# Kernel tuning notes

Measured on AMD Instinct MI355X. Metric: run time of the kernel, lower is better.

Reference implementation:

```python
import jax, jax.numpy as jnp
import numpy as np

B, P, D = 16384, 4096, 256

def setup_inputs() -> dict:
    key = jax.random.key(0)
    kx, kp = jax.random.split(key)
    x = jax.random.normal(kx, (B, D), dtype=jnp.float32)
    prototypes = jax.random.normal(kp, (P, D), dtype=jnp.float32)
    return {"x": x, "prototypes": prototypes}

def reference(x, prototypes):
    # Pairwise L2 distance: ||x - p||_2 for every (batch, prototype) pair.
    # GEMM reformulation avoids the O(B*P*D) broadcast intermediate:
    x_sq = jnp.sum(x * x, axis=-1, keepdims=True)                 # [B, 1]
    p_sq = jnp.sum(prototypes * prototypes, axis=-1)[None, :]     # [1, P]
    xp = jnp.einsum('bd,pd->bp', x, prototypes)                   # [B, P]
    sq_dist = jnp.maximum(x_sq + p_sq - 2.0 * xp, 0.0)
    return jnp.sqrt(sq_dist)                                      # [B, P]
```

## Files before the change

kernel.cpp:

```cpp
#include <hip/hip_runtime.h>
#include <hip/hip_bf16.h>

#define B_DIM 16384
#define P_DIM 4096
#define D_DIM 256
#define BK 32
#define NSTEP (D_DIM / BK)

typedef float f32x4 __attribute__((ext_vector_type(4)));
typedef __bf16 bf16x8 __attribute__((ext_vector_type(8)));

__device__ __forceinline__ unsigned short f2bf_rne(float f) {
  unsigned int u = __builtin_bit_cast(unsigned int, f);
  u += 0x7fffu + ((u >> 16) & 1u);
  return (unsigned short)(u >> 16);
}

__global__ __launch_bounds__(256) void prep_kernel(
    const float* __restrict__ x, const float* __restrict__ p,
    unsigned short* __restrict__ xb, unsigned short* __restrict__ pb,
    float* __restrict__ xsq, float* __restrict__ psq) {
  int row  = blockIdx.x * 4 + (threadIdx.x >> 6);
  int lane = threadIdx.x & 63;
  const float4* src;
  unsigned short* dst;
  float* sq;
  if (row < B_DIM) {
    src = (const float4*)(x + (size_t)row * D_DIM);
    dst = xb + (size_t)row * D_DIM;
    sq  = xsq + row;
  } else {
    int r = row - B_DIM;
    src = (const float4*)(p + (size_t)r * D_DIM);
    dst = pb + (size_t)r * D_DIM;
    sq  = psq + r;
  }
  float4 v = src[lane];
  ushort4 o;
  o.x = f2bf_rne(v.x); o.y = f2bf_rne(v.y);
  o.z = f2bf_rne(v.z); o.w = f2bf_rne(v.w);
  ((ushort4*)dst)[lane] = o;
  float s = v.x * v.x + v.y * v.y + v.z * v.z + v.w * v.w;
  #pragma unroll
  for (int off = 32; off > 0; off >>= 1) s += __shfl_down(s, off);
  if (lane == 0) *sq = s;
}

__device__ __forceinline__ void async16(const unsigned short* g, const void* l) {
  __builtin_amdgcn_global_load_lds(
      (const __attribute__((address_space(1))) void*)g,
      (__attribute__((address_space(3))) void*)l,
      16, 0, 0);
}

__global__ __launch_bounds__(256, 3) void dist_gemm(
    const unsigned short* __restrict__ A,
    const unsigned short* __restrict__ Bm,
    const float* __restrict__ xsq, const float* __restrict__ psq,
    float* __restrict__ out) {
  __shared__ __align__(16) char lds[3][2][8192];

  const int tid  = threadIdx.x;
  const int w    = tid >> 6;
  const int lane = tid & 63;
  const int bid  = blockIdx.x;

  const int swz = (bid & 7) * 512 + (bid >> 3);
  const int bm  = swz >> 5;
  const int bn  = swz & 31;

  const int wr = w >> 1;
  const int wc = w & 1;

  const int trow = tid >> 2;
  const int tcol = (((tid & 3) ^ (trow & 3)) << 3);
  const unsigned short* aSrc = A  + (size_t)(bm * 128 + trow) * D_DIM + tcol;
  const unsigned short* bSrc = Bm + (size_t)(bn * 128 + trow) * D_DIM + tcol;
  const int ldst = tid * 16;

#define STAGE(bufi, ktE) do { _Pragma("unroll")                                \
    for (int i = 0; i < 2; ++i) {                                              \
      async16(aSrc + (size_t)i * 64 * D_DIM + (ktE),                           \
              (const void*)(&lds[bufi][0][0] + i * 4096 + ldst));              \
      async16(bSrc + (size_t)i * 64 * D_DIM + (ktE),                           \
              (const void*)(&lds[bufi][1][0] + i * 4096 + ldst));              \
    } } while (0)

  const int arow = wr * 64 + (lane & 15);
  const int brow = wc * 64 + (lane & 15);
  const int koff = (((lane >> 4) ^ (lane & 3)) << 4);

  f32x4 acc[4][4];
  #pragma unroll
  for (int m = 0; m < 4; ++m)
    #pragma unroll
    for (int n = 0; n < 4; ++n) acc[m][n] = 0.0f;

  STAGE(0, 0);
  STAGE(1, BK);

  #pragma unroll
  for (int t = 0; t < NSTEP; ++t) {
    if (t < NSTEP - 1) asm volatile("s_waitcnt vmcnt(4)" ::: "memory");
    else               asm volatile("s_waitcnt vmcnt(0)" ::: "memory");
    __builtin_amdgcn_s_barrier();
    __builtin_amdgcn_sched_barrier(0);

    if (t < NSTEP - 2) {
      const int nb = (t + 2) % 3;
      STAGE(nb, (t + 2) * BK);
    }

    const char* La = &lds[t % 3][0][0];
    const char* Lb = &lds[t % 3][1][0];
    bf16x8 av[4], bv[4];
    #pragma unroll
    for (int m = 0; m < 4; ++m)
      av[m] = *(const bf16x8*)(La + (arow + m * 16) * 64 + koff);
    #pragma unroll
    for (int n = 0; n < 4; ++n)
      bv[n] = *(const bf16x8*)(Lb + (brow + n * 16) * 64 + koff);
    #pragma unroll
    for (int m = 0; m < 4; ++m)
      #pragma unroll
      for (int n = 0; n < 4; ++n)
        acc[m][n] = __builtin_amdgcn_mfma_f32_16x16x32_bf16(bv[n], av[m], acc[m][n], 0, 0, 0);
  }

  const int xrowB = bm * 128 + wr * 64;
  const int pcolB = bn * 128 + wc * 64;
  const int rL = lane & 15;
  const int hL = lane >> 4;

  f32x4 ps[4];
  #pragma unroll
  for (int n = 0; n < 4; ++n)
    ps[n] = *(const f32x4*)(psq + pcolB + n * 16 + hL * 4);

  #pragma unroll
  for (int m = 0; m < 4; ++m) {
    const float xs = xsq[xrowB + m * 16 + rL];
    float* orow = out + (size_t)(xrowB + m * 16 + rL) * P_DIM + pcolB + hL * 4;
    #pragma unroll
    for (int n = 0; n < 4; ++n) {
      f32x4 v;
      #pragma unroll
      for (int j = 0; j < 4; ++j) {
        float d = fmaf(-2.0f, acc[m][n][j], xs + ps[n][j]);
        v[j] = __builtin_sqrtf(fmaxf(d, 0.0f));
      }
      *(f32x4*)(orow + n * 16) = v;
    }
  }
#undef STAGE
}

extern "C" void kernel_launch(void* const* d_in, const int* in_sizes, int n_in,
                              void* d_out, int out_size, void* d_ws, size_t ws_size,
                              hipStream_t stream) {
  const float* x = (const float*)d_in[0];
  const float* p = (const float*)d_in[1];
  float* out = (float*)d_out;

  char* ws = (char*)d_ws;
  unsigned short* xb = (unsigned short*)ws;
  unsigned short* pb = (unsigned short*)(ws + (size_t)B_DIM * D_DIM * 2);
  float* xsq = (float*)(ws + (size_t)(B_DIM + P_DIM) * D_DIM * 2);
  float* psq = xsq + B_DIM;

  prep_kernel<<<(B_DIM + P_DIM) / 4, 256, 0, stream>>>(x, p, xb, pb, xsq, psq);

  dist_gemm<<<(B_DIM / 128) * (P_DIM / 128), 256, 0, stream>>>(xb, pb, xsq, psq, out);
}
```

Measured before the change: 92.47 us.

## Give each wave private LDS tiles to eliminate block-wide barriers

Each wave now stages its own 64-row A and B slices into a private double-buffered LDS region. Because no wave reads another wave's data, the s_barrier in the K loop is removed and only vmcnt waits remain. The cost is duplicated global loads, since A and B rows are each fetched by two waves, and twice the LDS per block (64KB). Occupancy is lowered to 2 blocks per CU to fit this, and the swizzle pattern is changed to match the new per-wave layout.

New measurement: 105.3 us. +13.8%, slower.

```diff
diff --git a/kernel.cpp b/kernel.cpp
--- a/kernel.cpp
+++ b/kernel.cpp
@@ -53,12 +53,12 @@
       16, 0, 0);
 }
 
-__global__ __launch_bounds__(256, 3) void dist_gemm(
+__global__ __launch_bounds__(256, 2) void dist_gemm(
     const unsigned short* __restrict__ A,
     const unsigned short* __restrict__ Bm,
     const float* __restrict__ xsq, const float* __restrict__ psq,
     float* __restrict__ out) {
-  __shared__ __align__(16) char lds[3][2][8192];
+  __shared__ __align__(16) char lds[4][2][2][4096];
 
   const int tid  = threadIdx.x;
   const int w    = tid >> 6;
@@ -71,24 +71,24 @@
 
   const int wr = w >> 1;
   const int wc = w & 1;
+  const int arowB = bm * 128 + wr * 64;
+  const int browB = bn * 128 + wc * 64;
 
-  const int trow = tid >> 2;
-  const int tcol = (((tid & 3) ^ (trow & 3)) << 3);
-  const unsigned short* aSrc = A  + (size_t)(bm * 128 + trow) * D_DIM + tcol;
-  const unsigned short* bSrc = Bm + (size_t)(bn * 128 + trow) * D_DIM + tcol;
-  const int ldst = tid * 16;
+  const int srow   = lane >> 2;
+  const int schunk = (lane & 3) ^ ((srow >> 1) & 3);
+  const unsigned short* aS = A  + (size_t)(arowB + srow) * D_DIM + schunk * 8;
+  const unsigned short* bS = Bm + (size_t)(browB + srow) * D_DIM + schunk * 8;
 
 #define STAGE(bufi, ktE) do { _Pragma("unroll")                                \
-    for (int i = 0; i < 2; ++i) {                                              \
-      async16(aSrc + (size_t)i * 64 * D_DIM + (ktE),                           \
-              (const void*)(&lds[bufi][0][0] + i * 4096 + ldst));              \
-      async16(bSrc + (size_t)i * 64 * D_DIM + (ktE),                           \
-              (const void*)(&lds[bufi][1][0] + i * 4096 + ldst));              \
+    for (int i = 0; i < 4; ++i) {                                              \
+      async16(aS + (size_t)i * 16 * D_DIM + (ktE),                             \
+              (const void*)(&lds[w][bufi][0][i * 1024 + lane * 16]));          \
+      async16(bS + (size_t)i * 16 * D_DIM + (ktE),                             \
+              (const void*)(&lds[w][bufi][1][i * 1024 + lane * 16]));          \
     } } while (0)
 
-  const int arow = wr * 64 + (lane & 15);
-  const int brow = wc * 64 + (lane & 15);
-  const int koff = (((lane >> 4) ^ (lane & 3)) << 4);
+  const int rl   = lane & 15;
+  const int koff = ((lane >> 4) ^ ((rl >> 1) & 3)) << 4;
 
   f32x4 acc[4][4];
   #pragma unroll
@@ -97,50 +97,43 @@
     for (int n = 0; n < 4; ++n) acc[m][n] = 0.0f;
 
   STAGE(0, 0);
-  STAGE(1, BK);
+  __builtin_amdgcn_sched_barrier(0);
 
   #pragma unroll
   for (int t = 0; t < NSTEP; ++t) {
-    if (t < NSTEP - 1) asm volatile("s_waitcnt vmcnt(4)" ::: "memory");
+    if (t < NSTEP - 1) STAGE((t + 1) & 1, (t + 1) * BK);
+    __builtin_amdgcn_sched_barrier(0);
+    if (t < NSTEP - 1) asm volatile("s_waitcnt vmcnt(8)" ::: "memory");
     else               asm volatile("s_waitcnt vmcnt(0)" ::: "memory");
-    __builtin_amdgcn_s_barrier();
     __builtin_amdgcn_sched_barrier(0);
 
-    if (t < NSTEP - 2) {
-      const int nb = (t + 2) % 3;
-      STAGE(nb, (t + 2) * BK);
-    }
-
-    const char* La = &lds[t % 3][0][0];
-    const char* Lb = &lds[t % 3][1][0];
+    const char* La = &lds[w][t & 1][0][0];
+    const char* Lb = &lds[w][t & 1][1][0];
     bf16x8 av[4], bv[4];
     #pragma unroll
     for (int m = 0; m < 4; ++m)
-      av[m] = *(const bf16x8*)(La + (arow + m * 16) * 64 + koff);
+      av[m] = *(const bf16x8*)(La + (m * 16 + rl) * 64 + koff);
     #pragma unroll
     for (int n = 0; n < 4; ++n)
-      bv[n] = *(const bf16x8*)(Lb + (brow + n * 16) * 64 + koff);
+      bv[n] = *(const bf16x8*)(Lb + (n * 16 + rl) * 64 + koff);
     #pragma unroll
     for (int m = 0; m < 4; ++m)
       #pragma unroll
       for (int n = 0; n < 4; ++n)
         acc[m][n] = __builtin_amdgcn_mfma_f32_16x16x32_bf16(bv[n], av[m], acc[m][n], 0, 0, 0);
+    __builtin_amdgcn_sched_barrier(0);
   }
 
-  const int xrowB = bm * 128 + wr * 64;
-  const int pcolB = bn * 128 + wc * 64;
-  const int rL = lane & 15;
   const int hL = lane >> 4;
-
   f32x4 ps[4];
   #pragma unroll
   for (int n = 0; n < 4; ++n)
-    ps[n] = *(const f32x4*)(psq + pcolB + n * 16 + hL * 4);
+    ps[n] = *(const f32x4*)(psq + browB + n * 16 + hL * 4);
 
   #pragma unroll
   for (int m = 0; m < 4; ++m) {
-    const float xs = xsq[xrowB + m * 16 + rL];
-    float* orow = out + (size_t)(xrowB + m * 16 + rL) * P_DIM + pcolB + hL * 4;
+    const float xs = xsq[arowB + m * 16 + rl];
+    float* orow = out + (size_t)(arowB + m * 16 + rl) * P_DIM + browB + hL * 4;
     #pragma unroll
     for (int n = 0; n < 4; ++n) {
       f32x4 v;
```
